# Kernel optimization log

Hardware: AMD Instinct MI355X
Metric: run time of the kernel (lower is better)

Reference implementation:

```python
import jax, jax.numpy as jnp
import numpy as np

TEMP = 0.01            # entropy temperature
THRESH = 0.92          # hamming similarity threshold
BETA = 0.25            # commitment weight
ENT_W = 0.1            # entropy loss weight


def _l2_normalize(x, axis=-1, eps=1e-12):
    n = jnp.sqrt(jnp.sum(x * x, axis=axis, keepdims=True))
    return x / jnp.maximum(n, eps)


def _entropy_loss(affinity):
    # affinity: [N, K] codebook affinities (cosine similarities)
    fa = affinity / TEMP
    probs = jax.nn.softmax(fa, axis=-1)
    log_probs = jax.nn.log_softmax(fa + 1e-5, axis=-1)
    avg_probs = jnp.mean(probs, axis=0)
    avg_entropy = -jnp.sum(avg_probs * jnp.log(avg_probs + 1e-5))
    sample_entropy = -jnp.mean(jnp.sum(probs * log_probs, axis=-1))
    return sample_entropy - avg_entropy


def _hamming_consistency_loss(input_blocks, z_e):
    # binary occupancy: non-air voxels -> 1
    binary = (jnp.argmax(input_blocks, axis=1) != 0).astype(jnp.float32)  # [B,24,24,24]
    B = binary.shape[0]
    # faithful to torch: plain reshapes (no transpose)
    patterns = binary.reshape(B, 6, 4, 6, 4, 6, 4).reshape(B, 6, 6, 6, 64).reshape(-1, 64)
    N = patterns.shape[0]
    P = patterns
    # pairwise hamming distance via two Gram matmuls
    ham = P @ (1.0 - P).T + (1.0 - P) @ P.T          # [N,N]
    sim = 1.0 - ham / 64.0
    mask = (sim > THRESH) & (~jnp.eye(N, dtype=bool))
    W = jax.lax.stop_gradient(jnp.where(mask, sim, 0.0))  # detached weights
    # pre-quant embeddings per chunk, l2-normalized; cosine distance matrix
    emb = jnp.transpose(z_e, (0, 2, 3, 4, 1)).reshape(N, -1)  # [N, C]
    en = _l2_normalize(emb, axis=1)
    cos = en @ en.T                                   # [N,N]
    dist = 1.0 - cos
    return jnp.sum(dist * W) / (jnp.sum(W) + 1e-8)


def setup_inputs() -> dict:
    key = jax.random.key(0)
    k1, k2, k3 = jax.random.split(key, 3)
    input_blocks = jax.random.normal(k1, (16, 32, 24, 24, 24), dtype=jnp.float32)
    z_e = jax.random.normal(k2, (16, 256, 6, 6, 6), dtype=jnp.float32)
    codebook = jax.random.normal(k3, (1024, 256), dtype=jnp.float32)
    return {"input_blocks": input_blocks, "z_e": z_e, "codebook": codebook}


def reference(input_blocks, z_e, codebook):
    B, C, H, W, D = z_e.shape
    z = jnp.transpose(z_e, (0, 2, 3, 4, 1)).reshape(-1, C)   # [N, C]
    zn = _l2_normalize(z, axis=1)
    en = _l2_normalize(codebook, axis=1)                      # [K, C]
    affinity = zn @ en.T                                      # [N, K]
    idx = jnp.argmax(affinity, axis=1)                        # max cosine == min L2 on sphere
    z_q = en[idx]                                             # [N, C]
    sg = jax.lax.stop_gradient
    codebook_loss = jnp.mean((z_q - sg(zn)) ** 2)
    commit_loss = BETA * jnp.mean((sg(z_q) - zn) ** 2)
    ent_loss = ENT_W * _entropy_loss(affinity)
    ham_loss = _hamming_consistency_loss(input_blocks, z_e)
    loss = codebook_loss + commit_loss + ent_loss + ham_loss
    # straight-through estimator
    z_q_ste = zn + sg(z_q - zn)
    z_q_out = jnp.transpose(z_q_ste.reshape(B, H, W, D, C), (0, 4, 1, 2, 3))
    return z_q_out, loss, idx
```

## Files before the change

kernel.cpp:

```cpp
#include <hip/hip_runtime.h>
#include <cstdint>
#include <cstddef>

#define N_ROWS 3456
#define C_DIM 256
#define K_CB 1024
#define B_SZ 16
#define SPATIAL 216
#define VOX 13824
#define NCH 32
#define NSB 216

typedef __attribute__((ext_vector_type(16))) float f32x16;
typedef __attribute__((ext_vector_type(8))) short bf16x8;

__device__ __forceinline__ unsigned short f2bf_rne(float f) {
    unsigned int u = __float_as_uint(f);
    u += 0x7FFFu + ((u >> 16) & 1u);
    return (unsigned short)(u >> 16);
}
__device__ __forceinline__ float bf2f(unsigned short h) {
    unsigned int u = ((unsigned int)h) << 16;
    return __uint_as_float(u);
}

__device__ __forceinline__ size_t swz(int n, int c) {
    return (size_t)(n >> 5) * 8192 + (size_t)((c >> 3) * 256) + (size_t)((n & 31) * 8) + (c & 7);
}

__global__ __launch_bounds__(256) void k_pre(
        const float* __restrict__ in, const float* __restrict__ cb,
        const float* __restrict__ ze,
        unsigned long long* __restrict__ pats,
        float* __restrict__ scal,
        float* __restrict__ en,
        unsigned short* __restrict__ ehi, unsigned short* __restrict__ elo,
        unsigned short* __restrict__ zhi, unsigned short* __restrict__ zlo) {
    int bid = blockIdx.x;
    int t = threadIdx.x;
    if (bid < 864) {
        if (bid == 0 && t < 16) scal[t] = 0.0f;
        int v = bid * 256 + t;
        int b = v / VOX;
        int r = v % VOX;
        const float* p = in + (size_t)b * NCH * VOX + r;
        float v0 = p[0];
        float mx = -INFINITY;
#pragma unroll
        for (int c = 1; c < NCH; ++c) mx = fmaxf(mx, p[(size_t)c * VOX]);
        unsigned long long m = __ballot(mx > v0);
        if ((t & 63) == 0) pats[v >> 6] = m;
        return;
    }
    __shared__ float ws[4];
    if (bid < 1888) {
        int k = bid - 864, c = t;
        float v = cb[k * C_DIM + c];
        float ss = v * v;
#pragma unroll
        for (int off = 32; off > 0; off >>= 1) ss += __shfl_down(ss, off, 64);
        if ((c & 63) == 0) ws[c >> 6] = ss;
        __syncthreads();
        float nrm = fmaxf(sqrtf(ws[0] + ws[1] + ws[2] + ws[3]), 1e-12f);
        float o = v / nrm;
        en[k * C_DIM + c] = o;
        unsigned short h = f2bf_rne(o);
        size_t off = swz(k, c);
        ehi[off] = h;
        elo[off] = f2bf_rne(o - bf2f(h));
    } else {
        int n = bid - 1888, c = t;
        int b = n / SPATIAL, s = n % SPATIAL;
        float v = ze[((size_t)(b * C_DIM + c)) * SPATIAL + s];
        float ss = v * v;
#pragma unroll
        for (int off = 32; off > 0; off >>= 1) ss += __shfl_down(ss, off, 64);
        if ((c & 63) == 0) ws[c >> 6] = ss;
        __syncthreads();
        float nrm = fmaxf(sqrtf(ws[0] + ws[1] + ws[2] + ws[3]), 1e-12f);
        float o = v / nrm;
        unsigned short h = f2bf_rne(o);
        size_t off = swz(n, c);
        zhi[off] = h;
        zlo[off] = f2bf_rne(o - bf2f(h));
    }
}

__global__ __launch_bounds__(128) void k_mid(
        const unsigned short* __restrict__ zhi, const unsigned short* __restrict__ zlo,
        const unsigned short* __restrict__ ehi, const unsigned short* __restrict__ elo,
        const unsigned long long* __restrict__ pats,
        float* __restrict__ aff, float* __restrict__ scal) {
    int t = threadIdx.x;
    int w = t >> 6, lane = t & 63;
    int bid = blockIdx.x;
    const bf16x8* __restrict__ Zh = (const bf16x8*)zhi;
    const bf16x8* __restrict__ Zl = (const bf16x8*)zlo;
    const bf16x8* __restrict__ Eh = (const bf16x8*)ehi;
    const bf16x8* __restrict__ El = (const bf16x8*)elo;

    if (bid < 432) {
        int ib = bid % 54, jb = bid / 54;
        int i0 = ib * 64, j0 = jb * 128;
        int sa = ib * 2;
        int sb = jb * 4 + w * 2;

        f32x16 acc[2][2];
#pragma unroll
        for (int r = 0; r < 2; ++r)
#pragma unroll
            for (int q = 0; q < 2; ++q)
#pragma unroll
                for (int e = 0; e < 16; ++e) acc[r][q][e] = 0.0f;

#pragma unroll
        for (int s16 = 0; s16 < 16; ++s16) {
            int u = s16 * 64 + lane;
            bf16x8 ah[2], al[2], bh[2], bl[2];
#pragma unroll
            for (int r = 0; r < 2; ++r) {
                ah[r] = Zh[(size_t)(sa + r) * 1024 + u];
                al[r] = Zl[(size_t)(sa + r) * 1024 + u];
            }
#pragma unroll
            for (int q = 0; q < 2; ++q) {
                bh[q] = Eh[(size_t)(sb + q) * 1024 + u];
                bl[q] = El[(size_t)(sb + q) * 1024 + u];
            }
#pragma unroll
            for (int r = 0; r < 2; ++r)
#pragma unroll
                for (int q = 0; q < 2; ++q) {
                    acc[r][q] = __builtin_amdgcn_mfma_f32_32x32x16_bf16(ah[r], bh[q], acc[r][q], 0, 0, 0);
                    acc[r][q] = __builtin_amdgcn_mfma_f32_32x32x16_bf16(ah[r], bl[q], acc[r][q], 0, 0, 0);
                    acc[r][q] = __builtin_amdgcn_mfma_f32_32x32x16_bf16(al[r], bh[q], acc[r][q], 0, 0, 0);
                }
        }
#pragma unroll
        for (int r = 0; r < 2; ++r)
#pragma unroll
            for (int q = 0; q < 2; ++q)
#pragma unroll
                for (int g = 0; g < 16; ++g) {
                    int row = i0 + r * 32 + (g & 3) + 8 * (g >> 2) + 4 * (lane >> 5);
                    int col = j0 + w * 64 + q * 32 + (lane & 31);
                    aff[(size_t)row * K_CB + col] = acc[r][q][g];
                }
        return;
    }

    int hb = bid - 432;
    int ti = 0, rem = hb;
    while (rem >= 27 - ti) { rem -= 27 - ti; ++ti; }
    int tj = ti + rem;
    int i0 = ti * 128, j0 = tj * 128;
    float factor = (ti == tj) ? 1.0f : 2.0f;
    int si = ti * 4 + w * 2;
    int sj = tj * 4;

    f32x16 acc[2][4];
#pragma unroll
    for (int a = 0; a < 2; ++a)
#pragma unroll
        for (int b = 0; b < 4; ++b)
#pragma unroll
            for (int e = 0; e < 16; ++e) acc[a][b][e] = 0.0f;

#pragma unroll
    for (int s16 = 0; s16 < 16; ++s16) {
        int u = s16 * 64 + lane;
        bf16x8 a0 = Zh[(size_t)si * 1024 + u];
        bf16x8 a1 = Zh[(size_t)(si + 1) * 1024 + u];
        bf16x8 bf[4];
#pragma unroll
        for (int c = 0; c < 4; ++c)
            bf[c] = Zh[(size_t)(sj + c) * 1024 + u];
#pragma unroll
        for (int c = 0; c < 4; ++c) {
            acc[0][c] = __builtin_amdgcn_mfma_f32_32x32x16_bf16(a0, bf[c], acc[0][c], 0, 0, 0);
            acc[1][c] = __builtin_amdgcn_mfma_f32_32x32x16_bf16(a1, bf[c], acc[1][c], 0, 0, 0);
        }
    }

    unsigned long long pj[4];
#pragma unroll
    for (int c = 0; c < 4; ++c) pj[c] = pats[j0 + c * 32 + (lane & 31)];

    float sW = 0.0f, sD = 0.0f;
#pragma unroll
    for (int r = 0; r < 2; ++r) {
        int ibase = i0 + w * 64 + r * 32 + 4 * (lane >> 5);
#pragma unroll
        for (int g = 0; g < 16; ++g) {
            int gi = ibase + (g & 3) + 8 * (g >> 2);
            unsigned long long pi = pats[gi];
#pragma unroll
            for (int c = 0; c < 4; ++c) {
                int gj = j0 + c * 32 + (lane & 31);
                int pop = __popcll(pi ^ pj[c]);
                float wgt = (pop <= 5 && gi != gj) ? (1.0f - (float)pop * 0.015625f) : 0.0f;
                sW += wgt;
                sD += wgt * acc[r][c][g];
            }
        }
    }
#pragma unroll
    for (int off = 32; off > 0; off >>= 1) {
        sW += __shfl_down(sW, off, 64);
        sD += __shfl_down(sD, off, 64);
    }
    if (lane == 0) {
        atomicAdd(&scal[2], factor * sW);
        atomicAdd(&scal[3], factor * sD);
    }
}

#define ZQS 257
__global__ __launch_bounds__(256) void k_post(
        const float* __restrict__ aff, const float* __restrict__ en,
        float* __restrict__ avgp_part, float* __restrict__ scal,
        float* __restrict__ out) {
    __shared__ float lps[4][K_CB];
    __shared__ float zq[16 * ZQS];
    __shared__ float lsc[8];
    __shared__ float ws4[4];
    __shared__ int lastflag;
    unsigned int* done = (unsigned int*)&scal[8];
    int t = threadIdx.x;
    int lane = t & 63, w = t >> 6;
    int n0 = blockIdx.x * 16;

    float ps[16];
#pragma unroll
    for (int i = 0; i < 16; ++i) ps[i] = 0.0f;
    float se = 0.0f, cm = 0.0f;

#pragma unroll
    for (int r = 0; r < 4; ++r) {
        int lr = w * 4 + r;
        int row = n0 + lr;
        const float* ap = aff + (size_t)row * K_CB;
        float4 v[4];
#pragma unroll
        for (int j = 0; j < 4; ++j)
            v[j] = *(const float4*)&ap[j * 256 + lane * 4];

        float m = v[0].x; int mi = lane * 4;
#pragma unroll
        for (int j = 0; j < 4; ++j)
#pragma unroll
            for (int i = 0; i < 4; ++i) {
                float x = ((const float*)&v[j])[i];
                int col = j * 256 + lane * 4 + i;
                if (x > m) { m = x; mi = col; }
            }
#pragma unroll
        for (int off = 32; off > 0; off >>= 1) {
            float vo = __shfl_down(m, off, 64);
            int   io = __shfl_down(mi, off, 64);
            if (vo > m || (vo == m && io < mi)) { m = vo; mi = io; }
        }
        m = __shfl(m, 0, 64);
        mi = __shfl(mi, 0, 64);

        float e[16];
        float S = 0.0f, T = 0.0f;
#pragma unroll
        for (int j = 0; j < 4; ++j)
#pragma unroll
            for (int i = 0; i < 4; ++i) {
                float d = 100.0f * (((const float*)&v[j])[i] - m);
                float ee = __expf(d);
                e[j * 4 + i] = ee; S += ee; T += ee * d;
            }
#pragma unroll
        for (int off = 32; off > 0; off >>= 1) {
            S += __shfl_down(S, off, 64);
            T += __shfl_down(T, off, 64);
        }
        S = __shfl(S, 0, 64);
        T = __shfl(T, 0, 64);
        float invS = 1.0f / S;
#pragma unroll
        for (int i = 0; i < 16; ++i) ps[i] += e[i] * invS;
        se += logf(S) - T * invS;
        cm += 2.0f - 2.0f * m;
        if (lane == 0) out[884737 + row] = (float)mi;

        float4 g4 = *(const float4*)&en[(size_t)mi * C_DIM + lane * 4];
        zq[lr * ZQS + lane * 4 + 0] = g4.x;
        zq[lr * ZQS + lane * 4 + 1] = g4.y;
        zq[lr * ZQS + lane * 4 + 2] = g4.z;
        zq[lr * ZQS + lane * 4 + 3] = g4.w;
    }

#pragma unroll
    for (int j = 0; j < 4; ++j)
#pragma unroll
        for (int i = 0; i < 4; ++i)
            lps[w][j * 256 + lane * 4 + i] = ps[j * 4 + i];
    if (lane == 0) { lsc[w] = se; lsc[4 + w] = cm; }
    __syncthreads();
#pragma unroll
    for (int c = 0; c < 4; ++c) {
        int col = t * 4 + c;
        avgp_part[(size_t)blockIdx.x * K_CB + col] =
            lps[0][col] + lps[1][col] + lps[2][col] + lps[3][col];
    }
    if (t == 0) atomicAdd(&scal[0], lsc[0] + lsc[1] + lsc[2] + lsc[3]);
    if (t == 1) atomicAdd(&scal[1], lsc[4] + lsc[5] + lsc[6] + lsc[7]);

    {
        int rlane = t & 15, cgrp = t >> 4;
        int n = n0 + rlane;
        int b = n / SPATIAL, s = n - b * SPATIAL;
        size_t obase = ((size_t)b * C_DIM) * SPATIAL + s;
#pragma unroll
        for (int cc = 0; cc < 16; ++cc) {
            int c = cgrp * 16 + cc;
            out[obase + (size_t)c * SPATIAL] = zq[rlane * ZQS + c];
        }
    }

    __syncthreads();
    if (t == 0) {
        __threadfence();
        unsigned int old = atomicAdd(done, 1u);
        lastflag = (old == NSB - 1) ? 1 : 0;
    }
    __syncthreads();
    if (lastflag) {
        __threadfence();
        float4 apv = make_float4(0.0f, 0.0f, 0.0f, 0.0f);
        for (int bb = 0; bb < NSB; ++bb) {
            float4 pv = *(const float4*)&avgp_part[(size_t)bb * K_CB + t * 4];
            apv.x += pv.x; apv.y += pv.y; apv.z += pv.z; apv.w += pv.w;
        }
        float term = 0.0f;
#pragma unroll
        for (int i = 0; i < 4; ++i) {
            float ap = ((const float*)&apv)[i] * (1.0f / N_ROWS);
            term += ap * logf(ap + 1e-5f);
        }
#pragma unroll
        for (int off = 32; off > 0; off >>= 1) term += __shfl_down(term, off, 64);
        if ((t & 63) == 0) ws4[t >> 6] = term;
        __syncthreads();
        if (t == 0) {
            float sAP = ws4[0] + ws4[1] + ws4[2] + ws4[3];
            float s0 = atomicAdd(&scal[0], 0.0f);
            float s1 = atomicAdd(&scal[1], 0.0f);
            float s2 = atomicAdd(&scal[2], 0.0f);
            float s3 = atomicAdd(&scal[3], 0.0f);
            float sample = s0 * (1.0f / N_ROWS);
            float commit = s1 * (1.0f / ((float)N_ROWS * C_DIM));
            float ent = 0.1f * (sample + sAP);
            float ham = (s2 - s3) / (s2 + 1e-8f);
            out[884736] = 1.25f * commit + ent + ham;
        }
    }
}

extern "C" void kernel_launch(void* const* d_in, const int* in_sizes, int n_in,
                              void* d_out, int out_size, void* d_ws, size_t ws_size,
                              hipStream_t stream) {
    const float* in_blocks = (const float*)d_in[0];
    const float* z_e       = (const float*)d_in[1];
    const float* cb        = (const float*)d_in[2];
    float* out = (float*)d_out;

    char* ws = (char*)d_ws;
    float* en   = (float*)(ws + 0);
    float* aff  = (float*)(ws + 1048576);
    unsigned short* zhi = (unsigned short*)(ws + 15204352);
    unsigned short* zlo = (unsigned short*)(ws + 16973824);
    unsigned short* ehi = (unsigned short*)(ws + 18743296);
    unsigned short* elo = (unsigned short*)(ws + 19267584);
    unsigned long long* pats = (unsigned long long*)(ws + 19791872);
    float* avgp_part = (float*)(ws + 19819520);
    float* scal = (float*)(ws + 20704256);

    k_pre<<<5344, 256, 0, stream>>>(in_blocks, cb, z_e, pats, scal,
                                    en, ehi, elo, zhi, zlo);
    k_mid<<<810, 128, 0, stream>>>(zhi, zlo, ehi, elo, pats, aff, scal);
    k_post<<<NSB, 256, 0, stream>>>(aff, en, avgp_part, scal, out);
}
```

Before: 152.7 us.

## Spread k_post over more blocks and accumulate avg probs with atomics

k_post now handles four rows per block (one per wave) instead of sixteen, so the grid grows from 216 to 864 blocks to fill more compute units. The per-block partial avg-prob buffer and the serial 216-way final reduction in the last block are replaced by global float atomicAdds into a 1024-entry array that k_pre zeroes. This trades more atomic traffic (1024 atomics per block, across 864 blocks) for better occupancy and a shorter tail in the last block. The float summation order also becomes nondeterministic.

```diff
diff --git a/kernel.cpp b/kernel.cpp
--- a/kernel.cpp
+++ b/kernel.cpp
@@ -9,7 +9,7 @@
 #define SPATIAL 216
 #define VOX 13824
 #define NCH 32
-#define NSB 216
+#define NSB 864
 
 typedef __attribute__((ext_vector_type(16))) float f32x16;
 typedef __attribute__((ext_vector_type(8))) short bf16x8;
@@ -33,13 +33,18 @@
         const float* __restrict__ ze,
         unsigned long long* __restrict__ pats,
         float* __restrict__ scal,
+        float* __restrict__ avgp,
         float* __restrict__ en,
         unsigned short* __restrict__ ehi, unsigned short* __restrict__ elo,
         unsigned short* __restrict__ zhi, unsigned short* __restrict__ zlo) {
     int bid = blockIdx.x;
     int t = threadIdx.x;
     if (bid < 864) {
-        if (bid == 0 && t < 16) scal[t] = 0.0f;
+        if (bid == 0) {
+            if (t < 16) scal[t] = 0.0f;
+#pragma unroll
+            for (int c = 0; c < 4; ++c) avgp[t * 4 + c] = 0.0f;
+        }
         int v = bid * 256 + t;
         int b = v / VOX;
         int r = v % VOX;
@@ -218,106 +223,94 @@
 #define ZQS 257
 __global__ __launch_bounds__(256) void k_post(
         const float* __restrict__ aff, const float* __restrict__ en,
-        float* __restrict__ avgp_part, float* __restrict__ scal,
+        float* __restrict__ avgp, float* __restrict__ scal,
         float* __restrict__ out) {
     __shared__ float lps[4][K_CB];
-    __shared__ float zq[16 * ZQS];
+    __shared__ float zq[4 * ZQS];
     __shared__ float lsc[8];
     __shared__ float ws4[4];
     __shared__ int lastflag;
     unsigned int* done = (unsigned int*)&scal[8];
     int t = threadIdx.x;
     int lane = t & 63, w = t >> 6;
-    int n0 = blockIdx.x * 16;
-
-    float ps[16];
-#pragma unroll
-    for (int i = 0; i < 16; ++i) ps[i] = 0.0f;
-    float se = 0.0f, cm = 0.0f;
-
-#pragma unroll
-    for (int r = 0; r < 4; ++r) {
-        int lr = w * 4 + r;
-        int row = n0 + lr;
-        const float* ap = aff + (size_t)row * K_CB;
-        float4 v[4];
-#pragma unroll
-        for (int j = 0; j < 4; ++j)
-            v[j] = *(const float4*)&ap[j * 256 + lane * 4];
-
-        float m = v[0].x; int mi = lane * 4;
-#pragma unroll
-        for (int j = 0; j < 4; ++j)
-#pragma unroll
-            for (int i = 0; i < 4; ++i) {
-                float x = ((const float*)&v[j])[i];
-                int col = j * 256 + lane * 4 + i;
-                if (x > m) { m = x; mi = col; }
-            }
-#pragma unroll
-        for (int off = 32; off > 0; off >>= 1) {
-            float vo = __shfl_down(m, off, 64);
-            int   io = __shfl_down(mi, off, 64);
-            if (vo > m || (vo == m && io < mi)) { m = vo; mi = io; }
-        }
-        m = __shfl(m, 0, 64);
-        mi = __shfl(mi, 0, 64);
-
-        float e[16];
-        float S = 0.0f, T = 0.0f;
-#pragma unroll
-        for (int j = 0; j < 4; ++j)
-#pragma unroll
-            for (int i = 0; i < 4; ++i) {
-                float d = 100.0f * (((const float*)&v[j])[i] - m);
-                float ee = __expf(d);
-                e[j * 4 + i] = ee; S += ee; T += ee * d;
-            }
-#pragma unroll
-        for (int off = 32; off > 0; off >>= 1) {
-            S += __shfl_down(S, off, 64);
-            T += __shfl_down(T, off, 64);
-        }
-        S = __shfl(S, 0, 64);
-        T = __shfl(T, 0, 64);
-        float invS = 1.0f / S;
-#pragma unroll
-        for (int i = 0; i < 16; ++i) ps[i] += e[i] * invS;
-        se += logf(S) - T * invS;
-        cm += 2.0f - 2.0f * m;
-        if (lane == 0) out[884737 + row] = (float)mi;
-
-        float4 g4 = *(const float4*)&en[(size_t)mi * C_DIM + lane * 4];
-        zq[lr * ZQS + lane * 4 + 0] = g4.x;
-        zq[lr * ZQS + lane * 4 + 1] = g4.y;
-        zq[lr * ZQS + lane * 4 + 2] = g4.z;
-        zq[lr * ZQS + lane * 4 + 3] = g4.w;
-    }
-
+    int n0 = blockIdx.x * 4;
+
+    int row = n0 + w;
+    const float* ap = aff + (size_t)row * K_CB;
+    float4 v[4];
 #pragma unroll
     for (int j = 0; j < 4; ++j)
+        v[j] = *(const float4*)&ap[j * 256 + lane * 4];
+
+    float m = v[0].x; int mi = lane * 4;
+#pragma unroll
+    for (int j = 0; j < 4; ++j)
+#pragma unroll
+        for (int i = 0; i < 4; ++i) {
+            float x = ((const float*)&v[j])[i];
+            int col = j * 256 + lane * 4 + i;
+            if (x > m) { m = x; mi = col; }
+        }
+#pragma unroll
+    for (int off = 32; off > 0; off >>= 1) {
+        float vo = __shfl_down(m, off, 64);
+        int   io = __shfl_down(mi, off, 64);
+        if (vo > m || (vo == m && io < mi)) { m = vo; mi = io; }
+    }
+    m = __shfl(m, 0, 64);
+    mi = __shfl(mi, 0, 64);
+
+    float e[16];
+    float S = 0.0f, T = 0.0f;
+#pragma unroll
+    for (int j = 0; j < 4; ++j)
+#pragma unroll
+        for (int i = 0; i < 4; ++i) {
+            float d = 100.0f * (((const float*)&v[j])[i] - m);
+            float ee = __expf(d);
+            e[j * 4 + i] = ee; S += ee; T += ee * d;
+        }
+#pragma unroll
+    for (int off = 32; off > 0; off >>= 1) {
+        S += __shfl_down(S, off, 64);
+        T += __shfl_down(T, off, 64);
+    }
+    S = __shfl(S, 0, 64);
+    T = __shfl(T, 0, 64);
+    float invS = 1.0f / S;
+    float se = logf(S) - T * invS;
+    float cm = 2.0f - 2.0f * m;
+    if (lane == 0) out[884737 + row] = (float)mi;
+
+    float4 g4 = *(const float4*)&en[(size_t)mi * C_DIM + lane * 4];
+    zq[w * ZQS + lane * 4 + 0] = g4.x;
+    zq[w * ZQS + lane * 4 + 1] = g4.y;
+    zq[w * ZQS + lane * 4 + 2] = g4.z;
+    zq[w * ZQS + lane * 4 + 3] = g4.w;
+
+#pragma unroll
+    for (int j = 0; j < 4; ++j)
 #pragma unroll
         for (int i = 0; i < 4; ++i)
-            lps[w][j * 256 + lane * 4 + i] = ps[j * 4 + i];
+            lps[w][j * 256 + lane * 4 + i] = e[j * 4 + i] * invS;
     if (lane == 0) { lsc[w] = se; lsc[4 + w] = cm; }
     __syncthreads();
 #pragma unroll
     for (int c = 0; c < 4; ++c) {
         int col = t * 4 + c;
-        avgp_part[(size_t)blockIdx.x * K_CB + col] =
-            lps[0][col] + lps[1][col] + lps[2][col] + lps[3][col];
+        atomicAdd(&avgp[col], lps[0][col] + lps[1][col] + lps[2][col] + lps[3][col]);
     }
     if (t == 0) atomicAdd(&scal[0], lsc[0] + lsc[1] + lsc[2] + lsc[3]);
     if (t == 1) atomicAdd(&scal[1], lsc[4] + lsc[5] + lsc[6] + lsc[7]);
 
     {
-        int rlane = t & 15, cgrp = t >> 4;
+        int rlane = t & 3, cgrp = t >> 2;
         int n = n0 + rlane;
         int b = n / SPATIAL, s = n - b * SPATIAL;
         size_t obase = ((size_t)b * C_DIM) * SPATIAL + s;
 #pragma unroll
-        for (int cc = 0; cc < 16; ++cc) {
-            int c = cgrp * 16 + cc;
+        for (int cc = 0; cc < 4; ++cc) {
+            int c = cgrp * 4 + cc;
             out[obase + (size_t)c * SPATIAL] = zq[rlane * ZQS + c];
         }
     }
@@ -331,16 +324,12 @@
     __syncthreads();
     if (lastflag) {
         __threadfence();
-        float4 apv = make_float4(0.0f, 0.0f, 0.0f, 0.0f);
-        for (int bb = 0; bb < NSB; ++bb) {
-            float4 pv = *(const float4*)&avgp_part[(size_t)bb * K_CB + t * 4];
-            apv.x += pv.x; apv.y += pv.y; apv.z += pv.z; apv.w += pv.w;
-        }
         float term = 0.0f;
 #pragma unroll
         for (int i = 0; i < 4; ++i) {
-            float ap = ((const float*)&apv)[i] * (1.0f / N_ROWS);
-            term += ap * logf(ap + 1e-5f);
+            float apv = atomicAdd(&avgp[t * 4 + i], 0.0f);
+            float ap2 = apv * (1.0f / N_ROWS);
+            term += ap2 * logf(ap2 + 1e-5f);
         }
 #pragma unroll
         for (int off = 32; off > 0; off >>= 1) term += __shfl_down(term, off, 64);
@@ -377,11 +366,11 @@
     unsigned short* ehi = (unsigned short*)(ws + 18743296);
     unsigned short* elo = (unsigned short*)(ws + 19267584);
     unsigned long long* pats = (unsigned long long*)(ws + 19791872);
-    float* avgp_part = (float*)(ws + 19819520);
+    float* avgp = (float*)(ws + 19819520);
     float* scal = (float*)(ws + 20704256);
 
-    k_pre<<<5344, 256, 0, stream>>>(in_blocks, cb, z_e, pats, scal,
+    k_pre<<<5344, 256, 0, stream>>>(in_blocks, cb, z_e, pats, scal, avgp,
                                     en, ehi, elo, zhi, zlo);
     k_mid<<<810, 128, 0, stream>>>(zhi, zlo, ehi, elo, pats, aff, scal);
-    k_post<<<NSB, 256, 0, stream>>>(aff, en, avgp_part, scal, out);
-}
+    k_post<<<NSB, 256, 0, stream>>>(aff, en, avgp, scal, out);
+}
```

Measured after the change: 229.7 us. +50.4%, slower.
